# Optimization experiments

Measured on AMD Instinct MI355X. Metric: run time of the kernel, lower is better.

Reference implementation:

```python
import jax, jax.numpy as jnp
import numpy as np

M, K, N, GROUP = 32, 8192, 28672, 128


def setup_inputs() -> dict:
    key = jax.random.key(0)
    k1, k2, k3, k4 = jax.random.split(key, 4)
    x = jax.random.normal(k1, (M, K), dtype=jnp.float16)
    # int32 words, each packing 8 consecutive int4 values along K
    qweight = jax.random.randint(k2, (K // 8, N), 0, 2147483647, dtype=jnp.int32)
    scales = (jax.random.uniform(k3, (K // GROUP, N), dtype=jnp.float32) * 0.01 + 0.001).astype(jnp.float16)
    bias = (jax.random.normal(k4, (N,), dtype=jnp.float32) * 0.02).astype(jnp.float16)
    return {"x": x, "qweight": qweight, "scales": scales, "bias": bias}


def reference(x, qweight, scales, bias):
    # Unpack 8 int4 nibbles per int32 word along K: (K//8, N) -> (K, N)
    K8, n = qweight.shape
    shifts = (jnp.arange(8, dtype=jnp.int32) * 4)[None, :, None]
    wq = ((qweight[:, None, :] >> shifts) & 15).reshape(K8 * 8, n)  # [K, N] in [0,15]
    # Dequant: zero-point fixed at 8 (pack() asserts zeros==8), per-group scales
    w = wq.astype(jnp.float16) - jnp.float16(8.0)
    g, gs = scales.shape[0], (K8 * 8) // scales.shape[0]
    w = (w.reshape(g, gs, n) * scales[:, None, :]).reshape(K8 * 8, n)  # [K, N] fp16
    return jnp.dot(x, w) + bias  # [M, N]
```

## Files before the change

### kernel.cpp

```cpp
#include <hip/hip_runtime.h>
#include <stdint.h>

#define K_DIM 8192
#define N_DIM 28672
#define NG    8

typedef _Float16 half8 __attribute__((ext_vector_type(8)));
typedef _Float16 half2t __attribute__((ext_vector_type(2)));
typedef float f32x16 __attribute__((ext_vector_type(16)));

__global__ __launch_bounds__(256) void prep_x(const float* __restrict__ x,
                                              _Float16* __restrict__ xp) {
  int idx = blockIdx.x * 256 + threadIdx.x;
  int m  = idx & 31;
  int k8 = idx >> 5;
  const float* p = x + (size_t)m * K_DIM + (size_t)k8 * 8;
  float4 xa = *(const float4*)p;
  float4 xb = *(const float4*)(p + 4);
  half2t p0 = __builtin_bit_cast(half2t, __builtin_amdgcn_cvt_pkrtz(xa.x, xb.x));
  half2t p1 = __builtin_bit_cast(half2t, __builtin_amdgcn_cvt_pkrtz(xa.y, xb.y));
  half2t p2 = __builtin_bit_cast(half2t, __builtin_amdgcn_cvt_pkrtz(xa.z, xb.z));
  half2t p3 = __builtin_bit_cast(half2t, __builtin_amdgcn_cvt_pkrtz(xa.w, xb.w));
  half8 o;
  o[0] = p0[0]; o[1] = p0[1]; o[2] = p1[0]; o[3] = p1[1];
  o[4] = p2[0]; o[5] = p2[1]; o[6] = p3[0]; o[7] = p3[1];
  *(half8*)(xp + ((size_t)k8 * 32 + m) * 8) = o;
}

static __device__ __forceinline__ half8 dqs(uint32_t w, half2t sh) {
  const uint32_t M4 = 0x000F000Fu, E = 0x64006400u;
  half2t off; off[0] = (_Float16)(-1032.0f); off[1] = (_Float16)(-1032.0f);
  half2t v0 = (__builtin_bit_cast(half2t, ( w        & M4) | E) + off) * sh;
  half2t v1 = (__builtin_bit_cast(half2t, ((w >> 4)  & M4) | E) + off) * sh;
  half2t v2 = (__builtin_bit_cast(half2t, ((w >> 8)  & M4) | E) + off) * sh;
  half2t v3 = (__builtin_bit_cast(half2t, ((w >> 12) & M4) | E) + off) * sh;
  half8 r;
  r[0] = v0[0]; r[1] = v0[1]; r[2] = v1[0]; r[3] = v1[1];
  r[4] = v2[0]; r[5] = v2[1]; r[6] = v3[0]; r[7] = v3[1];
  return r;
}

static __device__ __forceinline__ void waitcnt_vm8() { __builtin_amdgcn_s_waitcnt(0x0F78); }
static __device__ __forceinline__ void waitcnt_vm0() { __builtin_amdgcn_s_waitcnt(0x0F70); }

__global__ __launch_bounds__(512, 6) void qgemm(
    const uint32_t* __restrict__ q, const float* __restrict__ scales,
    const float* __restrict__ bias, const _Float16* __restrict__ xp,
    float* __restrict__ out) {
  __shared__ float red[8][16][64];
  const int tid  = threadIdx.x;
  const int w    = tid >> 6;
  const int lane = tid & 63;
  const int h    = lane >> 5;
  const int nl   = lane & 31;
  const int ct   = blockIdx.x;
  const int c0   = ct << 5;
  const int wr0  = w << 7;

  half2t sh[8];
#pragma unroll
  for (int g = 0; g < NG; g++) {
    float s = scales[(size_t)(w * NG + g) * N_DIM + c0 + nl];
    sh[g] = __builtin_bit_cast(half2t, __builtin_amdgcn_cvt_pkrtz(s, s));
  }
  waitcnt_vm0();
  __builtin_amdgcn_sched_barrier(0);

  const uint32_t qb = (uint32_t)((((uint64_t)(wr0 + h)) * N_DIM + c0 + nl) * 4);
  const uint32_t ab = (uint32_t)(((wr0 + h) * 32 + nl) * 16);

  uint32_t qr[2][8];
  float4   aA[8];

  auto qload = [&](int g, int p) {
#pragma unroll
    for (int i = 0; i < 8; i++) {
      uint32_t vo = qb + (uint32_t)(g * 16 + 2 * i) * (uint32_t)(N_DIM * 4);
      asm volatile("global_load_dword %0, %1, %2"
                   : "=v"(qr[p][i]) : "v"(vo), "s"(q));
    }
  };
  auto aload1 = [&](int g, int i) {
    uint32_t vo = ab + (uint32_t)(g * 8192 + i * 1024);
    asm volatile("global_load_dwordx4 %0, %1, %2"
                 : "=v"(aA[i]) : "v"(vo), "s"(xp));
  };

  f32x16 acc;
#pragma unroll
  for (int j = 0; j < 16; j++) acc[j] = 0.0f;

  qload(0, 0);
#pragma unroll
  for (int i = 0; i < 8; i++) aload1(0, i);
  qload(1, 1);

#pragma unroll
  for (int g = 0; g < NG; g++) {
    if (g < NG - 1) waitcnt_vm8(); else waitcnt_vm0();
    __builtin_amdgcn_sched_barrier(0);
    half2t s = sh[g];
#pragma unroll
    for (int i = 0; i < 8; i++) {
      acc = __builtin_amdgcn_mfma_f32_32x32x16_f16(
          __builtin_bit_cast(half8, aA[i]), dqs(qr[g & 1][i], s), acc, 0, 0, 0);
      if (g + 1 < NG) aload1(g + 1, i);
    }
    if (g + 2 < NG) qload(g + 2, g & 1);
  }

#pragma unroll
  for (int j = 0; j < 16; j++) red[w][j][lane] = acc[j];
  __syncthreads();

  float b = bias[c0 + nl];
#pragma unroll
  for (int jj = 0; jj < 2; jj++) {
    int j = w * 2 + jj;
    float v = red[0][j][lane] + red[1][j][lane] + red[2][j][lane] +
              red[3][j][lane] + red[4][j][lane] + red[5][j][lane] +
              red[6][j][lane] + red[7][j][lane];
    int row = (j & 3) + ((j >> 2) << 3) + (h << 2);
    out[(size_t)row * N_DIM + c0 + nl] = v + b;
  }
}

extern "C" void kernel_launch(void* const* d_in, const int* in_sizes, int n_in,
                              void* d_out, int out_size, void* d_ws, size_t ws_size,
                              hipStream_t stream) {
  const float*    xf      = (const float*)d_in[0];
  const uint32_t* qweight = (const uint32_t*)d_in[1];
  const float*    scales  = (const float*)d_in[2];
  const float*    bias    = (const float*)d_in[3];
  float*          out     = (float*)d_out;
  _Float16*       xp      = (_Float16*)d_ws;

  prep_x<<<dim3(128), dim3(256), 0, stream>>>(xf, xp);
  qgemm<<<dim3(N_DIM / 32), dim3(512), 0, stream>>>(qweight, scales, bias, xp, out);
}
```

Baseline: 215.7 us.

## Widen column tile to 64 per block with dwordx2 weight loads and two accumulators

Each block now covers 64 output columns instead of 32. Each lane loads two adjacent packed weight words with a single dwordx2 load and runs two MFMA chains that share the same activation fragment. This halves how often activations are reloaded per column and gives wider memory transactions. In exchange it halves the grid to 448 blocks, raises register use (occupancy hint lowered from 6 to 4), and runs the cross-wave reduction twice, with more LDS syncs and strided stores of alternating columns.

New measurement: 193.5 us. 10.3% less time.

```diff
diff --git a/kernel.cpp b/kernel.cpp
--- a/kernel.cpp
+++ b/kernel.cpp
@@ -8,6 +8,8 @@
 typedef _Float16 half8 __attribute__((ext_vector_type(8)));
 typedef _Float16 half2t __attribute__((ext_vector_type(2)));
 typedef float f32x16 __attribute__((ext_vector_type(16)));
+typedef float f32x4 __attribute__((ext_vector_type(4)));
+typedef uint32_t u32x2 __attribute__((ext_vector_type(2)));
 
 __global__ __launch_bounds__(256) void prep_x(const float* __restrict__ x,
                                               _Float16* __restrict__ xp) {
@@ -40,10 +42,14 @@
   return r;
 }
 
+static __device__ __forceinline__ half2t cvtp(float f) {
+  return __builtin_bit_cast(half2t, __builtin_amdgcn_cvt_pkrtz(f, f));
+}
+
 static __device__ __forceinline__ void waitcnt_vm8() { __builtin_amdgcn_s_waitcnt(0x0F78); }
 static __device__ __forceinline__ void waitcnt_vm0() { __builtin_amdgcn_s_waitcnt(0x0F70); }
 
-__global__ __launch_bounds__(512, 6) void qgemm(
+__global__ __launch_bounds__(512, 4) void qgemm(
     const uint32_t* __restrict__ q, const float* __restrict__ scales,
     const float* __restrict__ bias, const _Float16* __restrict__ xp,
     float* __restrict__ out) {
@@ -53,30 +59,32 @@
   const int lane = tid & 63;
   const int h    = lane >> 5;
   const int nl   = lane & 31;
-  const int ct   = blockIdx.x;
-  const int c0   = ct << 5;
+  const int c0   = blockIdx.x << 6;
   const int wr0  = w << 7;
 
-  half2t sh[8];
+  half2t sh[8][2];
 #pragma unroll
   for (int g = 0; g < NG; g++) {
-    float s = scales[(size_t)(w * NG + g) * N_DIM + c0 + nl];
-    sh[g] = __builtin_bit_cast(half2t, __builtin_amdgcn_cvt_pkrtz(s, s));
+#pragma unroll
+    for (int j = 0; j < 2; j++) {
+      float s = scales[(size_t)(w * NG + g) * N_DIM + c0 + 2 * nl + j];
+      sh[g][j] = cvtp(s);
+    }
   }
   waitcnt_vm0();
   __builtin_amdgcn_sched_barrier(0);
 
-  const uint32_t qb = (uint32_t)((((uint64_t)(wr0 + h)) * N_DIM + c0 + nl) * 4);
+  const uint32_t qb = (uint32_t)((((uint64_t)(wr0 + h)) * N_DIM + c0 + 2 * nl) * 4);
   const uint32_t ab = (uint32_t)(((wr0 + h) * 32 + nl) * 16);
 
-  uint32_t qr[2][8];
-  float4   aA[8];
+  u32x2 qr[2][8];
+  f32x4 aA[8];
 
   auto qload = [&](int g, int p) {
 #pragma unroll
     for (int i = 0; i < 8; i++) {
       uint32_t vo = qb + (uint32_t)(g * 16 + 2 * i) * (uint32_t)(N_DIM * 4);
-      asm volatile("global_load_dword %0, %1, %2"
+      asm volatile("global_load_dwordx2 %0, %1, %2"
                    : "=v"(qr[p][i]) : "v"(vo), "s"(q));
     }
   };
@@ -86,9 +94,9 @@
                  : "=v"(aA[i]) : "v"(vo), "s"(xp));
   };
 
-  f32x16 acc;
+  f32x16 acc0, acc1;
 #pragma unroll
-  for (int j = 0; j < 16; j++) acc[j] = 0.0f;
+  for (int j = 0; j < 16; j++) { acc0[j] = 0.f; acc1[j] = 0.f; }
 
   qload(0, 0);
 #pragma unroll
@@ -99,29 +107,38 @@
   for (int g = 0; g < NG; g++) {
     if (g < NG - 1) waitcnt_vm8(); else waitcnt_vm0();
     __builtin_amdgcn_sched_barrier(0);
-    half2t s = sh[g];
+    half2t s0 = sh[g][0], s1 = sh[g][1];
 #pragma unroll
     for (int i = 0; i < 8; i++) {
-      acc = __builtin_amdgcn_mfma_f32_32x32x16_f16(
-          __builtin_bit_cast(half8, aA[i]), dqs(qr[g & 1][i], s), acc, 0, 0, 0);
+      half8 af = __builtin_bit_cast(half8, aA[i]);
+      u32x2 qw = qr[g & 1][i];
+      acc0 = __builtin_amdgcn_mfma_f32_32x32x16_f16(af, dqs(qw[0], s0), acc0, 0, 0, 0);
+      acc1 = __builtin_amdgcn_mfma_f32_32x32x16_f16(af, dqs(qw[1], s1), acc1, 0, 0, 0);
       if (g + 1 < NG) aload1(g + 1, i);
     }
     if (g + 2 < NG) qload(g + 2, g & 1);
   }
 
+  float b0 = bias[c0 + 2 * nl];
+  (void)b0;
 #pragma unroll
-  for (int j = 0; j < 16; j++) red[w][j][lane] = acc[j];
-  __syncthreads();
-
-  float b = bias[c0 + nl];
+  for (int J = 0; J < 2; J++) {
+    f32x16 accJ = (J == 0) ? acc0 : acc1;
 #pragma unroll
-  for (int jj = 0; jj < 2; jj++) {
-    int j = w * 2 + jj;
-    float v = red[0][j][lane] + red[1][j][lane] + red[2][j][lane] +
-              red[3][j][lane] + red[4][j][lane] + red[5][j][lane] +
-              red[6][j][lane] + red[7][j][lane];
-    int row = (j & 3) + ((j >> 2) << 3) + (h << 2);
-    out[(size_t)row * N_DIM + c0 + nl] = v + b;
+    for (int r = 0; r < 16; r++) red[w][r][lane] = accJ[r];
+    __syncthreads();
+#pragma unroll
+    for (int s = 0; s < 2; s++) {
+      int p   = tid + s * 512;
+      int reg = p >> 6, ln = p & 63;
+      float v = 0.f;
+#pragma unroll
+      for (int u = 0; u < 8; u++) v += red[u][reg][ln];
+      int row = (reg & 3) + ((reg >> 2) << 3) + ((ln >> 5) << 2);
+      int col = c0 + 2 * (ln & 31) + J;
+      out[(size_t)row * N_DIM + col] = v + bias[col];
+    }
+    __syncthreads();
   }
 }
 
@@ -136,5 +153,5 @@
   _Float16*       xp      = (_Float16*)d_ws;
 
   prep_x<<<dim3(128), dim3(256), 0, stream>>>(xf, xp);
-  qgemm<<<dim3(N_DIM / 32), dim3(512), 0, stream>>>(qweight, scales, bias, xp, out);
+  qgemm<<<dim3(N_DIM / 64), dim3(512), 0, stream>>>(qweight, scales, bias, xp, out);
 }
```
